# Performance work log

Hardware: AMD Instinct MI355X
Metric: run time of the kernel (lower is better)

## Reference

```python
import jax, jax.numpy as jnp
import numpy as np

SIGMA = (1.0, 1.0, 1.0)
SIGMA_CUTOFF = 2.0


def _gauss1d(sigma, cutoff):
    radius = int(cutoff * float(sigma) + 0.5)
    if radius == 0:
        radius = 1
    x = np.arange(-radius, radius + 1, dtype=np.float32)
    phi = np.exp(-0.5 / (sigma * sigma) * x ** 2)
    return phi / phi.sum()


def _kernel3d(sigma, cutoff):
    k = _gauss1d(sigma, cutoff)
    k3 = np.einsum('i,j,k->ijk', k, k, k)
    k3 = k3 / k3.sum()
    return jnp.asarray(k3[None, None], dtype=jnp.float32)  # [1,1,k,k,k]


def setup_inputs() -> dict:
    key = jax.random.key(0)
    x = jax.random.normal(key, (1, 3, 256, 256, 256), dtype=jnp.float32)
    weight_x = _kernel3d(SIGMA[0], SIGMA_CUTOFF)
    weight_y = _kernel3d(SIGMA[1], SIGMA_CUTOFF)
    weight_z = _kernel3d(SIGMA[2], SIGMA_CUTOFF)
    return {"x": x, "weight_x": weight_x, "weight_y": weight_y, "weight_z": weight_z}


def reference(x, weight_x, weight_y, weight_z):
    # Per-channel (depthwise) 3D Gaussian smoothing with constant zero padding
    # of kernel_size//2, equivalent to SAME conv with odd kernel. The torch
    # module does 3 separate pad+conv3d calls; here fused into one grouped conv.
    w = jnp.concatenate([weight_x, weight_y, weight_z], axis=0)  # [3,1,k,k,k]
    k = w.shape[-1]
    p = k // 2
    out = jax.lax.conv_general_dilated(
        x, w,
        window_strides=(1, 1, 1),
        padding=[(p, p), (p, p), (p, p)],
        dimension_numbers=('NCDHW', 'OIDHW', 'NCDHW'),
        feature_group_count=3,
    )
    return out
```

## Files before the change

### kernel.cpp

```cpp
#include <hip/hip_runtime.h>


#define N    256
#define KS   5
#define R    2
#define TX   64
#define TY   16
#define TZ   32
#define ZB   4
#define NT   256
#define LROW 68
#define ROWS (TY + 4)
#define UPR  34
#define UNITS (ZB * ROWS * UPR)
#define MAXU ((UNITS + NT - 1) / NT)

__global__ __launch_bounds__(NT) void gauss3d_kernel(
    const float* __restrict__ xin,
    const float* __restrict__ wxp,
    const float* __restrict__ wyp,
    const float* __restrict__ wzp,
    float* __restrict__ out)
{
    __shared__ float raw[ZB][ROWS][LROW];
    __shared__ float k1[3][KS];

    const int tid = threadIdx.x;
    const int c   = blockIdx.z / (N / TZ);
    const int zt  = blockIdx.z % (N / TZ);
    const int x0  = blockIdx.x * TX;
    const int y0  = blockIdx.y * TY;
    const int z0  = zt * TZ;

    const float* w = (c == 0) ? wxp : (c == 1) ? wyp : wzp;

    if (tid < 3 * KS) {
        const int axis = tid / KS, idx = tid % KS;
        float s = 0.f;
        for (int a = 0; a < KS; ++a)
            for (int b = 0; b < KS; ++b) {
                int off;
                if (axis == 0)      off = idx * 25 + a * 5 + b;
                else if (axis == 1) off = a * 25 + idx * 5 + b;
                else                off = a * 25 + b * 5 + idx;
                s += w[off];
            }
        k1[axis][idx] = s;
    }
    __syncthreads();

    float kzr[KS], kyr[KS], kxr[KS];
#pragma unroll
    for (int i = 0; i < KS; ++i) {
        kzr[i] = k1[0][i];
        kyr[i] = k1[1][i];
        kxr[i] = k1[2][i];
    }

    const int iy = tid >> 4;
    const int ix = (tid & 15) << 2;

    float4 acc[KS];
#pragma unroll
    for (int j = 0; j < KS; ++j) acc[j] = make_float4(0.f, 0.f, 0.f, 0.f);

    const float* xc = xin + (size_t)c * N * N * N;
    float*       oc = out + (size_t)c * N * N * N;

    float* rawf = (float*)raw;

    for (int rnd = 0; rnd < (TZ + 2 * R) / ZB; ++rnd) {
        const int zb = z0 - R + rnd * ZB;

        __syncthreads();

        float2 v[MAXU];
#pragma unroll
        for (int i = 0; i < MAXU; ++i) {
            v[i] = make_float2(0.f, 0.f);
            const int u = tid + i * NT;
            if (u < UNITS) {
                const int rowi = u / UPR;
                const int j    = u - rowi * UPR;
                const int s    = rowi / ROWS;
                const int r    = rowi - s * ROWS;
                const int zs = zb + s;
                const int gy = y0 + r - R;
                const int gx = x0 - R + 2 * j;
                if ((unsigned)zs < (unsigned)N && (unsigned)gy < (unsigned)N &&
                    (unsigned)gx < (unsigned)N)
                    v[i] = *(const float2*)&xc[((size_t)zs * N + gy) * N + gx];
            }
        }
#pragma unroll
        for (int i = 0; i < MAXU; ++i) {
            const int u = tid + i * NT;
            if (u < UNITS)
                *(float2*)&rawf[2 * u] = v[i];
        }
        __syncthreads();

#pragma unroll
        for (int s = 0; s < ZB; ++s) {
            float4 yv = make_float4(0.f, 0.f, 0.f, 0.f);
#pragma unroll
            for (int h = 0; h < KS; ++h) {
                const float* rp = &raw[s][iy + h][ix];
                const float4 a = *(const float4*)rp;
                const float4 b = *(const float4*)(rp + 4);
                const float o0 = kxr[0]*a.x + kxr[1]*a.y + kxr[2]*a.z + kxr[3]*a.w + kxr[4]*b.x;
                const float o1 = kxr[0]*a.y + kxr[1]*a.z + kxr[2]*a.w + kxr[3]*b.x + kxr[4]*b.y;
                const float o2 = kxr[0]*a.z + kxr[1]*a.w + kxr[2]*b.x + kxr[3]*b.y + kxr[4]*b.z;
                const float o3 = kxr[0]*a.w + kxr[1]*b.x + kxr[2]*b.y + kxr[3]*b.z + kxr[4]*b.w;
                const float kh = kyr[h];
                yv.x += kh * o0; yv.y += kh * o1; yv.z += kh * o2; yv.w += kh * o3;
            }
#pragma unroll
            for (int j = 0; j < KS; ++j) {
                const float kj = kzr[4 - j];
                acc[j].x += kj * yv.x; acc[j].y += kj * yv.y;
                acc[j].z += kj * yv.z; acc[j].w += kj * yv.w;
            }
            const int zo = zb + s - R;
            if (zo >= z0) {
                *(float4*)&oc[((size_t)zo * N + (y0 + iy)) * N + (x0 + ix)] = acc[0];
            }
            acc[0] = acc[1]; acc[1] = acc[2]; acc[2] = acc[3]; acc[3] = acc[4];
            acc[4] = make_float4(0.f, 0.f, 0.f, 0.f);
        }
    }
}

extern "C" void kernel_launch(void* const* d_in, const int* in_sizes, int n_in,
                              void* d_out, int out_size, void* d_ws, size_t ws_size,
                              hipStream_t stream) {
    const float* x  = (const float*)d_in[0];
    const float* wx = (const float*)d_in[1];
    const float* wy = (const float*)d_in[2];
    const float* wz = (const float*)d_in[3];
    float* o = (float*)d_out;

    dim3 grid(N / TX, N / TY, 3 * (N / TZ));
    dim3 block(NT);
    gauss3d_kernel<<<grid, block, 0, stream>>>(x, wx, wy, wz, o);
}
```

Baseline: 371.3 us.

## Replace shared-memory tiling with per-wave full-row streaming through global loads

The shared-memory staging and block barriers are removed. Each wavefront now owns one full 256-wide y row and streams it along z, reading its 5 neighbouring rows (plus x halos) directly from global memory and relying on cache for reuse. The 1D kernel taps are taken from the central slices of the 3D weight and renormalised, rather than summed over the whole 3D weight. Outputs use nontemporal stores. This trades explicit LDS reuse for redundant global/L2 reads (each input row is read by 5 waves) in exchange for dropping barriers and LDS traffic.

Result: slower. 527.0 us (+41.9%).

```diff
diff --git a/kernel.cpp b/kernel.cpp
--- a/kernel.cpp
+++ b/kernel.cpp
@@ -1,19 +1,11 @@
 #include <hip/hip_runtime.h>
 
 
-#define N    256
-#define KS   5
-#define R    2
-#define TX   64
-#define TY   16
-#define TZ   32
-#define ZB   4
-#define NT   256
-#define LROW 68
-#define ROWS (TY + 4)
-#define UPR  34
-#define UNITS (ZB * ROWS * UPR)
-#define MAXU ((UNITS + NT - 1) / NT)
+#define N   256
+#define ZC  32
+#define NT  256
+
+typedef float f4n __attribute__((ext_vector_type(4)));
 
 __global__ __launch_bounds__(NT) void gauss3d_kernel(
     const float* __restrict__ xin,
@@ -22,112 +14,98 @@
     const float* __restrict__ wzp,
     float* __restrict__ out)
 {
-    __shared__ float raw[ZB][ROWS][LROW];
-    __shared__ float k1[3][KS];
+    const int tid  = threadIdx.x;
+    const int lane = tid & 63;
+    const int wid  = __builtin_amdgcn_readfirstlane(tid >> 6);
 
-    const int tid = threadIdx.x;
-    const int c   = blockIdx.z / (N / TZ);
-    const int zt  = blockIdx.z % (N / TZ);
-    const int x0  = blockIdx.x * TX;
-    const int y0  = blockIdx.y * TY;
-    const int z0  = zt * TZ;
+    const int c  = blockIdx.z;
+    const int y  = blockIdx.x * 4 + wid;
+    const int z0 = blockIdx.y * ZC;
+    const int gx = lane << 2;
 
-    const float* w = (c == 0) ? wxp : (c == 1) ? wyp : wzp;
+    const float* __restrict__ w = (c == 0) ? wxp : (c == 1) ? wyp : wzp;
 
-    if (tid < 3 * KS) {
-        const int axis = tid / KS, idx = tid % KS;
-        float s = 0.f;
-        for (int a = 0; a < KS; ++a)
-            for (int b = 0; b < KS; ++b) {
-                int off;
-                if (axis == 0)      off = idx * 25 + a * 5 + b;
-                else if (axis == 1) off = a * 25 + idx * 5 + b;
-                else                off = a * 25 + b * 5 + idx;
-                s += w[off];
-            }
-        k1[axis][idx] = s;
+    float kx[5], ky[5], kz[5];
+    float sx = 0.f, sy = 0.f, sz = 0.f;
+#pragma unroll
+    for (int i = 0; i < 5; ++i) {
+        kx[i] = w[60 + i];       sx += kx[i];
+        ky[i] = w[52 + 5 * i];   sy += ky[i];
+        kz[i] = w[25 * i + 12];  sz += kz[i];
     }
-    __syncthreads();
-
-    float kzr[KS], kyr[KS], kxr[KS];
+    const float rxs = 1.f / sx, rys = 1.f / sy, rzs = 1.f / sz;
 #pragma unroll
-    for (int i = 0; i < KS; ++i) {
-        kzr[i] = k1[0][i];
-        kyr[i] = k1[1][i];
-        kxr[i] = k1[2][i];
-    }
-
-    const int iy = tid >> 4;
-    const int ix = (tid & 15) << 2;
-
-    float4 acc[KS];
-#pragma unroll
-    for (int j = 0; j < KS; ++j) acc[j] = make_float4(0.f, 0.f, 0.f, 0.f);
+    for (int i = 0; i < 5; ++i) { kx[i] *= rxs; ky[i] *= rys; kz[i] *= rzs; }
 
     const float* xc = xin + (size_t)c * N * N * N;
     float*       oc = out + (size_t)c * N * N * N;
 
-    float* rawf = (float*)raw;
+    bool rok[5];
+    const float* rp[5];
+#pragma unroll
+    for (int h = 0; h < 5; ++h) {
+        const int gy = y + h - 2;
+        rok[h] = ((unsigned)gy < (unsigned)N);
+        const int gyc = rok[h] ? gy : 0;
+        rp[h] = xc + ((long)(z0 - 2) * N + gyc) * (long)N;
+    }
 
-    for (int rnd = 0; rnd < (TZ + 2 * R) / ZB; ++rnd) {
-        const int zb = z0 - R + rnd * ZB;
+    const bool le = (gx == 0);
+    const bool re = (gx == N - 4);
+    const int  il = le ? 0  : gx - 2;
+    const int  ir = re ? gx : gx + 4;
 
-        __syncthreads();
+    float4 a0 = make_float4(0.f, 0.f, 0.f, 0.f);
+    float4 a1 = a0, a2 = a0, a3 = a0, a4 = a0;
 
-        float2 v[MAXU];
+    float* op = oc + ((size_t)z0 * N + y) * N;
+
+    for (int t = 0; t < ZC + 4; ++t) {
+        const int  zs  = z0 - 2 + t;
+        const bool zok = ((unsigned)zs < (unsigned)N);
+
+        float4 yv = make_float4(0.f, 0.f, 0.f, 0.f);
 #pragma unroll
-        for (int i = 0; i < MAXU; ++i) {
-            v[i] = make_float2(0.f, 0.f);
-            const int u = tid + i * NT;
-            if (u < UNITS) {
-                const int rowi = u / UPR;
-                const int j    = u - rowi * UPR;
-                const int s    = rowi / ROWS;
-                const int r    = rowi - s * ROWS;
-                const int zs = zb + s;
-                const int gy = y0 + r - R;
-                const int gx = x0 - R + 2 * j;
-                if ((unsigned)zs < (unsigned)N && (unsigned)gy < (unsigned)N &&
-                    (unsigned)gx < (unsigned)N)
-                    v[i] = *(const float2*)&xc[((size_t)zs * N + gy) * N + gx];
+        for (int h = 0; h < 5; ++h) {
+            float4 v;  float2 lm, rm;
+            if (zok && rok[h]) {
+                lm = *(const float2*)(rp[h] + il);
+                v  = *(const float4*)(rp[h] + gx);
+                rm = *(const float2*)(rp[h] + ir);
+            } else {
+                lm = make_float2(0.f, 0.f);
+                v  = make_float4(0.f, 0.f, 0.f, 0.f);
+                rm = make_float2(0.f, 0.f);
             }
+            const float l0 = le ? 0.f : lm.x;
+            const float l1 = le ? 0.f : lm.y;
+            const float r0 = re ? 0.f : rm.x;
+            const float r1 = re ? 0.f : rm.y;
+            const float o0 = kx[0]*l0  + kx[1]*l1  + kx[2]*v.x + kx[3]*v.y + kx[4]*v.z;
+            const float o1 = kx[0]*l1  + kx[1]*v.x + kx[2]*v.y + kx[3]*v.z + kx[4]*v.w;
+            const float o2 = kx[0]*v.x + kx[1]*v.y + kx[2]*v.z + kx[3]*v.w + kx[4]*r0;
+            const float o3 = kx[0]*v.y + kx[1]*v.z + kx[2]*v.w + kx[3]*r0  + kx[4]*r1;
+            const float kh = ky[h];
+            yv.x += kh * o0; yv.y += kh * o1; yv.z += kh * o2; yv.w += kh * o3;
         }
-#pragma unroll
-        for (int i = 0; i < MAXU; ++i) {
-            const int u = tid + i * NT;
-            if (u < UNITS)
-                *(float2*)&rawf[2 * u] = v[i];
-        }
-        __syncthreads();
 
 #pragma unroll
-        for (int s = 0; s < ZB; ++s) {
-            float4 yv = make_float4(0.f, 0.f, 0.f, 0.f);
-#pragma unroll
-            for (int h = 0; h < KS; ++h) {
-                const float* rp = &raw[s][iy + h][ix];
-                const float4 a = *(const float4*)rp;
-                const float4 b = *(const float4*)(rp + 4);
-                const float o0 = kxr[0]*a.x + kxr[1]*a.y + kxr[2]*a.z + kxr[3]*a.w + kxr[4]*b.x;
-                const float o1 = kxr[0]*a.y + kxr[1]*a.z + kxr[2]*a.w + kxr[3]*b.x + kxr[4]*b.y;
-                const float o2 = kxr[0]*a.z + kxr[1]*a.w + kxr[2]*b.x + kxr[3]*b.y + kxr[4]*b.z;
-                const float o3 = kxr[0]*a.w + kxr[1]*b.x + kxr[2]*b.y + kxr[3]*b.z + kxr[4]*b.w;
-                const float kh = kyr[h];
-                yv.x += kh * o0; yv.y += kh * o1; yv.z += kh * o2; yv.w += kh * o3;
-            }
-#pragma unroll
-            for (int j = 0; j < KS; ++j) {
-                const float kj = kzr[4 - j];
-                acc[j].x += kj * yv.x; acc[j].y += kj * yv.y;
-                acc[j].z += kj * yv.z; acc[j].w += kj * yv.w;
-            }
-            const int zo = zb + s - R;
-            if (zo >= z0) {
-                *(float4*)&oc[((size_t)zo * N + (y0 + iy)) * N + (x0 + ix)] = acc[0];
-            }
-            acc[0] = acc[1]; acc[1] = acc[2]; acc[2] = acc[3]; acc[3] = acc[4];
-            acc[4] = make_float4(0.f, 0.f, 0.f, 0.f);
+        for (int h = 0; h < 5; ++h) rp[h] += N * N;
+
+        a0.x += kz[4]*yv.x; a0.y += kz[4]*yv.y; a0.z += kz[4]*yv.z; a0.w += kz[4]*yv.w;
+        a1.x += kz[3]*yv.x; a1.y += kz[3]*yv.y; a1.z += kz[3]*yv.z; a1.w += kz[3]*yv.w;
+        a2.x += kz[2]*yv.x; a2.y += kz[2]*yv.y; a2.z += kz[2]*yv.z; a2.w += kz[2]*yv.w;
+        a3.x += kz[1]*yv.x; a3.y += kz[1]*yv.y; a3.z += kz[1]*yv.z; a3.w += kz[1]*yv.w;
+        a4.x += kz[0]*yv.x; a4.y += kz[0]*yv.y; a4.z += kz[0]*yv.z; a4.w += kz[0]*yv.w;
+
+        if (t >= 4) {
+            f4n s;
+            s.x = a0.x; s.y = a0.y; s.z = a0.z; s.w = a0.w;
+            __builtin_nontemporal_store(s, (f4n*)(op + gx));
+            op += N * N;
         }
+        a0 = a1; a1 = a2; a2 = a3; a3 = a4;
+        a4 = make_float4(0.f, 0.f, 0.f, 0.f);
     }
 }
 
@@ -140,7 +118,7 @@
     const float* wz = (const float*)d_in[3];
     float* o = (float*)d_out;
 
-    dim3 grid(N / TX, N / TY, 3 * (N / TZ));
+    dim3 grid(N / 4, N / ZC, 3);
     dim3 block(NT);
     gauss3d_kernel<<<grid, block, 0, stream>>>(x, wx, wy, wz, o);
 }
```
